# Kernel tuning notes

Measured on AMD Instinct MI355X. Metric: run time of the kernel, lower is better.

Reference implementation:

```python
import jax, jax.numpy as jnp
import numpy as np


def setup_inputs() -> dict:
    key = jax.random.key(0)
    ks = jax.random.split(key, 3)
    B, d_in, d_latent = 8192, 768, 12288
    x = jax.random.normal(ks[0], (B, d_in), dtype=jnp.float32)
    # kaiming_normal fan_in relu: std = sqrt(2/d_in)
    W_enc = jax.random.normal(ks[1], (d_latent, d_in), dtype=jnp.float32) * np.sqrt(2.0 / d_in)
    b_enc = jnp.zeros((d_latent,), dtype=jnp.float32)
    # xavier_normal: std = sqrt(2/(d_in+d_latent))
    W_dec = jax.random.normal(ks[2], (d_in, d_latent), dtype=jnp.float32) * np.sqrt(2.0 / (d_in + d_latent))
    b_dec = jnp.zeros((d_in,), dtype=jnp.float32)
    b_pre = jnp.zeros((d_in,), dtype=jnp.float32)
    return {"x": x, "b_pre": b_pre, "W_enc": W_enc, "b_enc": b_enc,
            "W_dec": W_dec, "b_dec": b_dec, "k": 64}


def reference(x, b_pre, W_enc, b_enc, W_dec, b_dec, k):
    # encode: a = (x - b_pre) @ W_enc.T + b_enc   -> (B, d_latent)
    x0 = x - b_pre
    a = jnp.einsum('bi,li->bl', x0, W_enc) + b_enc
    # topk activation (mode='value', nonneg=True): relu then keep k largest
    a_relu = jax.nn.relu(a)
    topk_val, topk_idx = jax.lax.top_k(a_relu, k)  # (B, k)
    B = a.shape[0]
    rows = jnp.arange(B)[:, None]
    z = jnp.zeros_like(a).at[rows, topk_idx].set(topk_val)
    # decode: x_hat = z @ W_dec.T + b_dec
    x_hat = jnp.einsum('bl,il->bi', z, W_dec) + b_dec
    return (x_hat, z, a)
```

## Files before the change

### kernel.cpp

```cpp
#include <hip/hip_runtime.h>

#define DIN 768
#define DL  12288
#define CAP 320
#define CAP2 512
#define BCAP 2048
#define TCAND 2.9f
#define MARGIN 0.03f
#define UB 0.015f
#define UMAX 64
#define KMAX 128

typedef __attribute__((ext_vector_type(8))) _Float16 half8;
typedef __attribute__((ext_vector_type(4))) _Float16 half4v;
typedef __attribute__((ext_vector_type(4))) float f32x4;

__device__ __forceinline__ void gl_lds16(const void* g, void* s) {
  __builtin_amdgcn_global_load_lds(
      (const __attribute__((address_space(1))) unsigned int*)g,
      (__attribute__((address_space(3))) unsigned int*)s, 16, 0, 0);
}
__device__ __forceinline__ void wait_lgkm0_fence() {
  asm volatile("s_waitcnt lgkmcnt(0)" ::: "memory");
  __builtin_amdgcn_sched_barrier(0);
}
__device__ __forceinline__ void wait_vm0() {
  asm volatile("s_waitcnt vmcnt(0)" ::: "memory");
}

#define NBX (8192 * DIN / 1024)
#define NBW (DL * DIN / 1024)
#define NBT ((DL / 32) * (DIN / 32))

__global__ __launch_bounds__(256) void k_prep(
    const float* __restrict__ x, const float* __restrict__ b_pre,
    const float* __restrict__ W_enc, const float* __restrict__ W_dec,
    _Float16* __restrict__ Ah, _Float16* __restrict__ Bh, _Float16* __restrict__ WT)
{
  const int b = blockIdx.x, tid = threadIdx.x;
  if (b < NBX) {
    const int i4 = b * 256 + tid;
    const int col4 = (i4 % (DIN / 4)) * 4;
    const float4 xv = *(const float4*)&x[(size_t)i4 * 4];
    const float4 bp = *(const float4*)&b_pre[col4];
    half4v o;
    o.x = (_Float16)(xv.x - bp.x);
    o.y = (_Float16)(xv.y - bp.y);
    o.z = (_Float16)(xv.z - bp.z);
    o.w = (_Float16)(xv.w - bp.w);
    *(half4v*)&Ah[(size_t)i4 * 4] = o;
  } else if (b < NBX + NBW) {
    const int i4 = (b - NBX) * 256 + tid;
    const float4 wv = *(const float4*)&W_enc[(size_t)i4 * 4];
    half4v o;
    o.x = (_Float16)wv.x; o.y = (_Float16)wv.y;
    o.z = (_Float16)wv.z; o.w = (_Float16)wv.w;
    *(half4v*)&Bh[(size_t)i4 * 4] = o;
  } else {
    const int idx = b - NBX - NBW;
    const int c0 = (idx % (DL / 32)) * 32;
    const int r0 = (idx / (DL / 32)) * 32;
    const int xx = tid & 31, yy = tid >> 5;
    __shared__ float t[32][33];
#pragma unroll
    for (int dy = 0; dy < 32; dy += 8)
      t[yy + dy][xx] = W_dec[(size_t)(r0 + yy + dy) * DL + c0 + xx];
    __syncthreads();
#pragma unroll
    for (int dy = 0; dy < 32; dy += 8)
      WT[(size_t)(c0 + yy + dy) * DIN + r0 + xx] = (_Float16)t[xx][yy + dy];
  }
}

#define BM 256
#define BN 256
#define BKE 64
#define NKT (DIN / BKE)

template <int EMIT>
__global__ __launch_bounds__(512) void k_encode_f16(
    const _Float16* __restrict__ Ah, const _Float16* __restrict__ Bh,
    const float* __restrict__ b_enc, float* __restrict__ aout,
    int* __restrict__ cnt, int2* __restrict__ cand)
{
  __shared__ _Float16 sA[2][BM][BKE];
  __shared__ _Float16 sB[2][BN][BKE];
  __shared__ int s_bcnt;
  const int tid = threadIdx.x, wave = tid >> 6, lane = tid & 63;
  const int wm = wave >> 2, wn = wave & 3;
  const int fr = lane & 15, fc = lane >> 4;

  const int q = ((8192 / BM) * (DL / BN)) >> 3;
  const int wg = (blockIdx.x & 7) * q + (blockIdx.x >> 3);
  const int bm = (wg / (DL / BN)) * BM;
  const int bn = (wg % (DL / BN)) * BN;

  const int lrow = lane >> 3;
  const int lcol = ((lane & 7) ^ lrow) << 3;
  const _Float16* gA = Ah + (size_t)(bm + lrow) * DIN + lcol;
  const _Float16* gB = Bh + (size_t)(bn + lrow) * DIN + lcol;

  f32x4 acc[8][4];
#pragma unroll
  for (int i = 0; i < 8; ++i)
#pragma unroll
    for (int j = 0; j < 4; ++j) acc[i][j] = f32x4{0.f, 0.f, 0.f, 0.f};

#define STAGE_TILE(buf, tt)                                                      \
  {                                                                              \
    _Pragma("unroll")                                                            \
    for (int s4 = 0; s4 < 4; ++s4) {                                             \
      const int s8 = (wave + s4 * 8) * 8;                                        \
      gl_lds16(gA + (size_t)s8 * DIN + (tt) * BKE, &sA[buf][s8][0]);             \
      gl_lds16(gB + (size_t)s8 * DIN + (tt) * BKE, &sB[buf][s8][0]);             \
    }                                                                            \
  }

#define LOADQ(p, mh, nh)                                                         \
  {                                                                              \
    const char* bA = (const char*)&sA[p][0][0];                                  \
    const char* bB = (const char*)&sB[p][0][0];                                  \
    _Pragma("unroll")                                                            \
    for (int i = 0; i < 4; ++i)                                                  \
      _Pragma("unroll")                                                          \
      for (int ks = 0; ks < 2; ++ks) {                                           \
        const int row = wm * 128 + ((mh) * 4 + i) * 16 + fr;                     \
        const int ph = (ks * 4 + fc) ^ (fr & 7);                                 \
        af[i][ks] = *(const half8*)(bA + row * (BKE * 2) + ph * 16);             \
      }                                                                          \
    _Pragma("unroll")                                                            \
    for (int j = 0; j < 2; ++j)                                                  \
      _Pragma("unroll")                                                          \
      for (int ks = 0; ks < 2; ++ks) {                                           \
        const int row = wn * 64 + ((nh) * 2 + j) * 16 + fr;                      \
        const int ph = (ks * 4 + fc) ^ (fr & 7);                                 \
        bf[j][ks] = *(const half8*)(bB + row * (BKE * 2) + ph * 16);             \
      }                                                                          \
  }

#define MFMAQ(mh, nh)                                                            \
  __builtin_amdgcn_s_setprio(1);                                                 \
  _Pragma("unroll")                                                              \
  for (int i = 0; i < 4; ++i)                                                    \
    _Pragma("unroll")                                                            \
    for (int j = 0; j < 2; ++j)                                                  \
      _Pragma("unroll")                                                          \
      for (int ks = 0; ks < 2; ++ks)                                             \
        acc[(mh) * 4 + i][(nh) * 2 + j] = __builtin_amdgcn_mfma_f32_16x16x32_f16( \
            af[i][ks], bf[j][ks], acc[(mh) * 4 + i][(nh) * 2 + j], 0, 0, 0);     \
  __builtin_amdgcn_s_setprio(0);

  half8 af[4][2], bf[2][2];

  STAGE_TILE(0, 0)
  wait_vm0();
  __builtin_amdgcn_s_barrier();

#pragma unroll 1
  for (int t = 0; t < NKT; ++t) {
    const int p = t & 1;
    LOADQ(p, 0, 0)
    if (t + 1 < NKT) STAGE_TILE(p ^ 1, t + 1)
    __builtin_amdgcn_s_barrier();
    wait_lgkm0_fence();
    MFMAQ(0, 0)
    __builtin_amdgcn_s_barrier();
    LOADQ(p, 0, 1)
    __builtin_amdgcn_s_barrier();
    wait_lgkm0_fence();
    MFMAQ(0, 1)
    __builtin_amdgcn_s_barrier();
    LOADQ(p, 1, 0)
    __builtin_amdgcn_s_barrier();
    wait_lgkm0_fence();
    MFMAQ(1, 0)
    __builtin_amdgcn_s_barrier();
    LOADQ(p, 1, 1)
    wait_vm0();
    __builtin_amdgcn_s_barrier();
    wait_lgkm0_fence();
    MFMAQ(1, 1)
    __builtin_amdgcn_s_barrier();
  }

  unsigned* pk   = (unsigned*)&sA[0][0][0];
  float*    pv   = (float*)&sA[1][0][0];
  int*      lcnt = (int*)&sB[0][0][0];
  if (EMIT) {
    if (tid == 0) s_bcnt = 0;
    if (tid < 256) lcnt[tid] = 0;
    __syncthreads();
  }

#pragma unroll
  for (int j = 0; j < 4; ++j) {
    const int col = bn + wn * 64 + j * 16 + fr;
    const float be = b_enc[col];
#pragma unroll
    for (int i = 0; i < 8; ++i) {
      const int row0 = bm + wm * 128 + i * 16 + fc * 4;
#pragma unroll
      for (int r = 0; r < 4; ++r) {
        const float v = acc[i][j][r] + be;
        aout[(size_t)(row0 + r) * DL + col] = v;
        if (EMIT && v > TCAND) {
          const int lr = wm * 128 + i * 16 + fc * 4 + r;
          const int lc = wn * 64 + j * 16 + fr;
          const int p2 = atomicAdd(&s_bcnt, 1);
          if (p2 < BCAP) {
            pk[p2] = ((unsigned)lr << 8) | (unsigned)lc;
            pv[p2] = v;
          }
          atomicAdd(&lcnt[lr], 1);
        }
      }
    }
  }

  if (EMIT) {
    __syncthreads();
    const int total = s_bcnt;
    if (total > BCAP) {
      if (tid < 256) atomicAdd(&cnt[bm + tid], CAP2);
    } else {
      if (tid < 256) {
        const int c = lcnt[tid];
        lcnt[tid] = c ? atomicAdd(&cnt[bm + tid], c) : 0;
      }
      __syncthreads();
      for (int e = tid; e < total; e += 512) {
        const unsigned pkv = pk[e];
        const int lr = pkv >> 8, lc = pkv & 255u;
        const int p2 = atomicAdd(&lcnt[lr], 1);
        if (p2 < CAP2) {
          int2 o; o.x = __float_as_int(pv[e]); o.y = bn + lc;
          cand[(size_t)(bm + lr) * CAP2 + p2] = o;
        }
      }
    }
  }
#undef STAGE_TILE
#undef LOADQ
#undef MFMAQ
}

__global__ __launch_bounds__(512) void k_fast(
    const int* __restrict__ cnt, const int2* __restrict__ cand,
    const float* __restrict__ x, const float* __restrict__ b_pre,
    const float* __restrict__ W, const float* __restrict__ b_enc,
    const int* __restrict__ kp, const _Float16* __restrict__ WT,
    const float* __restrict__ b_dec, float* __restrict__ z,
    float* __restrict__ xhat, int* __restrict__ flag)
{
  const int row = blockIdx.x, tid = threadIdx.x;
  const int wave = tid >> 6, lane = tid & 63;
  const int kk = min(max(kp[0], 1), KMAX);
  float* zr = z + (size_t)row * DL;

  __shared__ float cv[CAP2];
  __shared__ int ci[CAP2];
  __shared__ double x0[DIN];
  __shared__ float s_ak;
  __shared__ int s_nw, s_ucnt;
  __shared__ int uidx[UMAX];
  __shared__ double uex[UMAX];
  __shared__ int widx[KMAX];
  __shared__ float wval[KMAX];

  const float4 zz = {0.f, 0.f, 0.f, 0.f};
#pragma unroll
  for (int j = 0; j < 6; ++j) ((float4*)zr)[tid + 512 * j] = zz;

  const int Craw = cnt[row];
  const int C = min(Craw, CAP2);
  for (int i = tid; i < C; i += 512) {
    const int2 p = cand[(size_t)row * CAP2 + i];
    cv[i] = __int_as_float(p.x);
    ci[i] = p.y;
  }
  for (int i = tid; i < DIN; i += 512)
    x0[i] = (double)x[(size_t)row * DIN + i] - (double)b_pre[i];
  if (tid == 0) { s_ak = -1e30f; s_nw = 0; s_ucnt = 0; }
  __syncthreads();

  bool defic = (Craw >= CAP2) || (C < kk);
  if (!defic) {
    if (tid < C) {
      const float mv = cv[tid];
      const int mi = ci[tid];
      int r = 0;
      for (int j = 0; j < C; ++j) {
        const float fj = cv[j];
        if (fj > mv || (fj == mv && ci[j] < mi)) ++r;
      }
      if (r == kk - 1) s_ak = mv;
    }
    __syncthreads();
    if (s_ak - UB <= TCAND) defic = true;
  } else {
    __syncthreads();
  }
  if (defic) {
    if (tid == 0) flag[row] = 1;
    return;
  }
  const float ak = s_ak;

  if (tid < C) {
    const float mv = cv[tid];
    if (mv > ak + UB) {
      const int p = atomicAdd(&s_nw, 1);
      widx[p] = ci[tid]; wval[p] = mv;
    } else if (mv >= ak - UB) {
      const int p = atomicAdd(&s_ucnt, 1);
      if (p < UMAX) uidx[p] = ci[tid];
    }
  }
  __syncthreads();
  const int nci = s_nw;
  const int ucnt = min(s_ucnt, UMAX);

  for (int c = wave; c < ucnt; c += 8) {
    const int idx = uidx[c];
    const float* wrow = W + (size_t)idx * DIN;
    double s = 0.0;
#pragma unroll
    for (int it = 0; it < DIN / 64; ++it)
      s = fma(x0[lane + it * 64], (double)wrow[lane + it * 64], s);
#pragma unroll
    for (int mm = 32; mm; mm >>= 1) s += __shfl_xor(s, mm);
    if (lane == 0) {
      const double e = s + (double)b_enc[idx];
      uex[c] = e > 0.0 ? e : 0.0;
    }
  }
  __syncthreads();

  const int utake = min(kk - nci, ucnt);
  if (tid < ucnt) {
    const double mv = uex[tid];
    const int mi = uidx[tid];
    int r = 0;
    for (int j = 0; j < ucnt; ++j) {
      const double fj = uex[j];
      if (fj > mv || (fj == mv && uidx[j] < mi)) ++r;
    }
    if (r < utake) {
      const int p = atomicAdd(&s_nw, 1);
      widx[p] = mi; wval[p] = (float)mv;
    }
  }
  __syncthreads();
  const int nW = s_nw;

  if (tid < nW) zr[widx[tid]] = wval[tid];

  if (tid < 192) {
    float4 acc = ((const float4*)b_dec)[tid];
    for (int j = 0; j < nW; ++j) {
      const float vv = wval[j];
      const half4v w4 = *(const half4v*)(WT + (size_t)widx[j] * DIN + tid * 4);
      acc.x = fmaf(vv, (float)w4.x, acc.x);
      acc.y = fmaf(vv, (float)w4.y, acc.y);
      acc.z = fmaf(vv, (float)w4.z, acc.z);
      acc.w = fmaf(vv, (float)w4.w, acc.w);
    }
    ((float4*)(xhat + (size_t)row * DIN))[tid] = acc;
  }
}

template <int FORCE_ALL, int ZERO_Z>
__global__ __launch_bounds__(512) void k_full(
    const float* __restrict__ a, const float* __restrict__ x,
    const float* __restrict__ b_pre, const float* __restrict__ W,
    const float* __restrict__ b_enc, const int* __restrict__ kp,
    const _Float16* __restrict__ WT, const float* __restrict__ b_dec,
    float* __restrict__ z, float* __restrict__ xhat, const int* __restrict__ flag)
{
  const int row = blockIdx.x, tid = threadIdx.x;
  if (!FORCE_ALL && flag[row] == 0) return;
  const int wave = tid >> 6, lane = tid & 63;
  const int kk = min(max(kp[0], 1), KMAX);
  const float* ar = a + (size_t)row * DL;
  float* zr = z + (size_t)row * DL;

  __shared__ unsigned hist[4][512];
  __shared__ float s_wmax[8];
  __shared__ unsigned s_wsuf[8];
  __shared__ float s_Tm;
  __shared__ int s_cnt;
  __shared__ int cidx[CAP];
  __shared__ float caf[CAP];
  __shared__ double x0[DIN];
  __shared__ float s_ak;
  __shared__ int s_ucnt, s_nw;
  __shared__ int uidx[UMAX];
  __shared__ double uex[UMAX];
  __shared__ int widx[KMAX];
  __shared__ float wval[KMAX];

  float4 v[6];
#pragma unroll
  for (int j = 0; j < 6; ++j) {
    float4 t4 = ((const float4*)ar)[tid + 512 * j];
    t4.x = fmaxf(t4.x, 0.f); t4.y = fmaxf(t4.y, 0.f);
    t4.z = fmaxf(t4.z, 0.f); t4.w = fmaxf(t4.w, 0.f);
    v[j] = t4;
    if (ZERO_Z) {
      const float4 zz = {0.f, 0.f, 0.f, 0.f};
      ((float4*)zr)[tid + 512 * j] = zz;
    }
  }
  for (int i = tid; i < DIN; i += 512)
    x0[i] = (double)x[(size_t)row * DIN + i] - (double)b_pre[i];
  float m = 0.f;
#pragma unroll
  for (int j = 0; j < 6; ++j)
    m = fmaxf(m, fmaxf(fmaxf(v[j].x, v[j].y), fmaxf(v[j].z, v[j].w)));
#pragma unroll
  for (int off = 32; off; off >>= 1) m = fmaxf(m, __shfl_xor(m, off));
  if (lane == 0) s_wmax[wave] = m;
  if (tid == 0) { s_cnt = 0; s_Tm = -1.f; s_ak = -1e30f; s_ucnt = 0; s_nw = 0; }
  __syncthreads();
  float rmax = s_wmax[0];
#pragma unroll
  for (int w2 = 1; w2 < 8; ++w2) rmax = fmaxf(rmax, s_wmax[w2]);

  float Tm;
  if (rmax <= 0.f) {
    Tm = 1e30f;
  } else {
    const float scale = 512.f / rmax;
    unsigned need = (unsigned)kk;
    bool found = false;
    for (int phase = 0; phase < 2 && !found; ++phase) {
      for (int i = tid; i < 4 * 512; i += 512) (&hist[0][0])[i] = 0u;
      __syncthreads();
      unsigned* h = hist[wave & 3];
      const float sc = (phase == 0) ? scale : scale * 8.f;
#pragma unroll
      for (int j = 0; j < 6; ++j) {
        const float vv[4] = {v[j].x, v[j].y, v[j].z, v[j].w};
#pragma unroll
        for (int e = 0; e < 4; ++e) {
          const float val = vv[e];
          if (val > 0.f) {
            const float fb = val * scale;
            if (phase == 0) {
              if (fb >= 64.f) atomicAdd(&h[min(511, (int)fb)], 1u);
            } else {
              if (fb < 64.f) atomicAdd(&h[min(511, (int)(val * sc))], 1u);
            }
          }
        }
      }
      __syncthreads();
      const unsigned st = hist[0][tid] + hist[1][tid] + hist[2][tid] + hist[3][tid];
      unsigned s = st;
#pragma unroll
      for (int off = 1; off < 64; off <<= 1) {
        const unsigned o = __shfl_down(s, off);
        if (lane + off < 64) s += o;
      }
      if (lane == 0) s_wsuf[wave] = s;
      __syncthreads();
      unsigned above_w = 0, total = 0;
#pragma unroll
      for (int w2 = 0; w2 < 8; ++w2) {
        total += s_wsuf[w2];
        if (w2 > wave) above_w += s_wsuf[w2];
      }
      const unsigned inc = s + above_w;
      const unsigned excl = inc - st;
      if (total >= need) {
        if (inc >= need && excl < need)
          s_Tm = (float)tid / sc - MARGIN;
        found = true;
      } else {
        need -= total;
      }
      __syncthreads();
    }
    Tm = s_Tm;
  }

#pragma unroll
  for (int j = 0; j < 6; ++j) {
    const float vv[4] = {v[j].x, v[j].y, v[j].z, v[j].w};
#pragma unroll
    for (int e = 0; e < 4; ++e) {
      if (vv[e] > 0.f && vv[e] >= Tm) {
        const int p = atomicAdd(&s_cnt, 1);
        if (p < CAP) { cidx[p] = (tid + 512 * j) * 4 + e; caf[p] = vv[e]; }
      }
    }
  }
  __syncthreads();
  const int C = min(s_cnt, CAP);

  if (C > kk) {
    if (tid < C) {
      const float mv = caf[tid];
      const int mi = cidx[tid];
      int r = 0;
      for (int j = 0; j < C; ++j) {
        const float fj = caf[j];
        if (fj > mv || (fj == mv && cidx[j] < mi)) ++r;
      }
      if (r == kk - 1) s_ak = mv;
    }
    __syncthreads();
  }
  const float ak = s_ak;

  if (tid < C) {
    const float mv = caf[tid];
    if (C <= kk || mv > ak + UB) {
      const int p = atomicAdd(&s_nw, 1);
      widx[p] = cidx[tid]; wval[p] = mv;
    } else if (mv >= ak - UB) {
      const int p = atomicAdd(&s_ucnt, 1);
      if (p < UMAX) uidx[p] = cidx[tid];
    }
  }
  __syncthreads();
  const int nci = s_nw;
  const int ucnt = min(s_ucnt, UMAX);

  for (int c = wave; c < ucnt; c += 8) {
    const int idx = uidx[c];
    const float* wrow = W + (size_t)idx * DIN;
    double s = 0.0;
#pragma unroll
    for (int it = 0; it < DIN / 64; ++it)
      s = fma(x0[lane + it * 64], (double)wrow[lane + it * 64], s);
#pragma unroll
    for (int mm = 32; mm; mm >>= 1) s += __shfl_xor(s, mm);
    if (lane == 0) {
      const double e = s + (double)b_enc[idx];
      uex[c] = e > 0.0 ? e : 0.0;
    }
  }
  __syncthreads();

  const int utake = min(kk - nci, ucnt);
  if (tid < ucnt) {
    const double mv = uex[tid];
    const int mi = uidx[tid];
    int r = 0;
    for (int j = 0; j < ucnt; ++j) {
      const double fj = uex[j];
      if (fj > mv || (fj == mv && uidx[j] < mi)) ++r;
    }
    if (r < utake) {
      const int p = atomicAdd(&s_nw, 1);
      widx[p] = mi; wval[p] = (float)mv;
    }
  }
  __syncthreads();
  const int nW = s_nw;

  if (tid < nW) zr[widx[tid]] = wval[tid];

  if (tid < 192) {
    float4 acc = ((const float4*)b_dec)[tid];
    for (int j = 0; j < nW; ++j) {
      const float vv = wval[j];
      const half4v w4 = *(const half4v*)(WT + (size_t)widx[j] * DIN + tid * 4);
      acc.x = fmaf(vv, (float)w4.x, acc.x);
      acc.y = fmaf(vv, (float)w4.y, acc.y);
      acc.z = fmaf(vv, (float)w4.z, acc.z);
      acc.w = fmaf(vv, (float)w4.w, acc.w);
    }
    ((float4*)(xhat + (size_t)row * DIN))[tid] = acc;
  }
}

extern "C" void kernel_launch(void* const* d_in, const int* in_sizes, int n_in,
                              void* d_out, int out_size, void* d_ws, size_t ws_size,
                              hipStream_t stream)
{
  const float* x     = (const float*)d_in[0];
  const float* b_pre = (const float*)d_in[1];
  const float* W_enc = (const float*)d_in[2];
  const float* b_enc = (const float*)d_in[3];
  const float* W_dec = (const float*)d_in[4];
  const float* b_dec = (const float*)d_in[5];
  const int*   kp    = (const int*)d_in[6];
  const int M = in_sizes[0] / DIN;

  float* xhat = (float*)d_out;
  float* z    = xhat + (size_t)M * DIN;
  float* a    = z + (size_t)M * DL;

  const bool bigws = ws_size >= ((size_t)192 << 20);

  if (bigws) {
    int*      cnt  = (int*)d_ws;
    int*      flag = (int*)d_ws + M;
    int2*     cand = (int2*)((char*)d_ws + ((size_t)1 << 20));
    _Float16* WT16 = (_Float16*)((char*)d_ws + ((size_t)40 << 20));
    _Float16* Ah   = (_Float16*)((char*)d_ws + ((size_t)64 << 20));
    _Float16* Bh   = (_Float16*)((char*)d_ws + ((size_t)96 << 20));

    hipMemsetAsync(d_ws, 0, 2 * M * sizeof(int), stream);
    k_prep<<<NBX + NBW + NBT, 256, 0, stream>>>(x, b_pre, W_enc, W_dec, Ah, Bh, WT16);
    k_encode_f16<1><<<(M / BM) * (DL / BN), 512, 0, stream>>>(Ah, Bh, b_enc, a, cnt, cand);
    k_fast<<<M, 512, 0, stream>>>(cnt, cand, x, b_pre, W_enc, b_enc, kp, WT16, b_dec,
                                  z, xhat, flag);
    k_full<0, 0><<<M, 512, 0, stream>>>(a, x, b_pre, W_enc, b_enc, kp, WT16, b_dec,
                                        z, xhat, flag);
  } else {
    _Float16* WT16 = (_Float16*)z;
    _Float16* Ah   = (_Float16*)(z + (size_t)12 * 1024 * 1024);
    _Float16* Bh   = (_Float16*)(z + (size_t)20 * 1024 * 1024);

    k_prep<<<NBX + NBW + NBT, 256, 0, stream>>>(x, b_pre, W_enc, W_dec, Ah, Bh, WT16);
    k_encode_f16<0><<<(M / BM) * (DL / BN), 512, 0, stream>>>(Ah, Bh, b_enc, a,
                                                              nullptr, nullptr);
    k_full<1, 1><<<M, 512, 0, stream>>>(a, x, b_pre, W_enc, b_enc, kp, WT16, b_dec,
                                        z, xhat, nullptr);
  }
}
```

Before: 661.2 us.

## Move z zeroing into encode GEMM prologue and fold counter memset into prep

The dense zeroing of z moves out of the per-row k_fast kernel. Each encode GEMM block now writes zeros for its own 256x256 tile of z during the prologue, overlapped with the first tile's global-to-LDS loads through a partial vmcnt wait. The separate hipMemsetAsync of the count/flag array is replaced by one extra k_prep block that zeroes it, removing an API call. The risk is that the GEMM's extra stores compete for bandwidth with its operand loads, and the vmcnt(32) wait must correctly cover the staged loads.

```diff
diff --git a/kernel.cpp b/kernel.cpp
--- a/kernel.cpp
+++ b/kernel.cpp
@@ -32,10 +32,12 @@
 #define NBW (DL * DIN / 1024)
 #define NBT ((DL / 32) * (DIN / 32))
 
+template <int ZMETA>
 __global__ __launch_bounds__(256) void k_prep(
     const float* __restrict__ x, const float* __restrict__ b_pre,
     const float* __restrict__ W_enc, const float* __restrict__ W_dec,
-    _Float16* __restrict__ Ah, _Float16* __restrict__ Bh, _Float16* __restrict__ WT)
+    _Float16* __restrict__ Ah, _Float16* __restrict__ Bh, _Float16* __restrict__ WT,
+    int* __restrict__ meta)
 {
   const int b = blockIdx.x, tid = threadIdx.x;
   if (b < NBX) {
@@ -56,7 +58,7 @@
     o.x = (_Float16)wv.x; o.y = (_Float16)wv.y;
     o.z = (_Float16)wv.z; o.w = (_Float16)wv.w;
     *(half4v*)&Bh[(size_t)i4 * 4] = o;
-  } else {
+  } else if (b < NBX + NBW + NBT) {
     const int idx = b - NBX - NBW;
     const int c0 = (idx % (DL / 32)) * 32;
     const int r0 = (idx / (DL / 32)) * 32;
@@ -69,6 +71,10 @@
 #pragma unroll
     for (int dy = 0; dy < 32; dy += 8)
       WT[(size_t)(c0 + yy + dy) * DIN + r0 + xx] = (_Float16)t[xx][yy + dy];
+  } else if (ZMETA) {
+    const int4 z4 = {0, 0, 0, 0};
+#pragma unroll
+    for (int s = 0; s < 16; ++s) ((int4*)meta)[tid * 16 + s] = z4;
   }
 }
 
@@ -81,7 +87,7 @@
 __global__ __launch_bounds__(512) void k_encode_f16(
     const _Float16* __restrict__ Ah, const _Float16* __restrict__ Bh,
     const float* __restrict__ b_enc, float* __restrict__ aout,
-    int* __restrict__ cnt, int2* __restrict__ cand)
+    int* __restrict__ cnt, int2* __restrict__ cand, float* __restrict__ zout)
 {
   __shared__ _Float16 sA[2][BM][BKE];
   __shared__ _Float16 sB[2][BN][BKE];
@@ -153,7 +159,15 @@
   half8 af[4][2], bf[2][2];
 
   STAGE_TILE(0, 0)
-  wait_vm0();
+  if (EMIT) {
+    const float4 zz4 = {0.f, 0.f, 0.f, 0.f};
+#pragma unroll
+    for (int s = 0; s < 32; ++s)
+      *(float4*)&zout[(size_t)(bm + s * 8 + wave) * DL + bn + lane * 4] = zz4;
+    asm volatile("s_waitcnt vmcnt(32)" ::: "memory");
+  } else {
+    wait_vm0();
+  }
   __builtin_amdgcn_s_barrier();
 
 #pragma unroll 1
@@ -266,10 +280,6 @@
   __shared__ double uex[UMAX];
   __shared__ int widx[KMAX];
   __shared__ float wval[KMAX];
-
-  const float4 zz = {0.f, 0.f, 0.f, 0.f};
-#pragma unroll
-  for (int j = 0; j < 6; ++j) ((float4*)zr)[tid + 512 * j] = zz;
 
   const int Craw = cnt[row];
   const int C = min(Craw, CAP2);
@@ -603,9 +613,10 @@
     _Float16* Ah   = (_Float16*)((char*)d_ws + ((size_t)64 << 20));
     _Float16* Bh   = (_Float16*)((char*)d_ws + ((size_t)96 << 20));
 
-    hipMemsetAsync(d_ws, 0, 2 * M * sizeof(int), stream);
-    k_prep<<<NBX + NBW + NBT, 256, 0, stream>>>(x, b_pre, W_enc, W_dec, Ah, Bh, WT16);
-    k_encode_f16<1><<<(M / BM) * (DL / BN), 512, 0, stream>>>(Ah, Bh, b_enc, a, cnt, cand);
+    k_prep<1><<<NBX + NBW + NBT + 1, 256, 0, stream>>>(x, b_pre, W_enc, W_dec,
+                                                       Ah, Bh, WT16, cnt);
+    k_encode_f16<1><<<(M / BM) * (DL / BN), 512, 0, stream>>>(Ah, Bh, b_enc, a,
+                                                              cnt, cand, z);
     k_fast<<<M, 512, 0, stream>>>(cnt, cand, x, b_pre, W_enc, b_enc, kp, WT16, b_dec,
                                   z, xhat, flag);
     k_full<0, 0><<<M, 512, 0, stream>>>(a, x, b_pre, W_enc, b_enc, kp, WT16, b_dec,
@@ -615,9 +626,10 @@
     _Float16* Ah   = (_Float16*)(z + (size_t)12 * 1024 * 1024);
     _Float16* Bh   = (_Float16*)(z + (size_t)20 * 1024 * 1024);
 
-    k_prep<<<NBX + NBW + NBT, 256, 0, stream>>>(x, b_pre, W_enc, W_dec, Ah, Bh, WT16);
+    k_prep<0><<<NBX + NBW + NBT, 256, 0, stream>>>(x, b_pre, W_enc, W_dec,
+                                                   Ah, Bh, WT16, nullptr);
     k_encode_f16<0><<<(M / BM) * (DL / BN), 512, 0, stream>>>(Ah, Bh, b_enc, a,
-                                                              nullptr, nullptr);
+                                                              nullptr, nullptr, nullptr);
     k_full<1, 1><<<M, 512, 0, stream>>>(a, x, b_pre, W_enc, b_enc, kp, WT16, b_dec,
                                         z, xhat, nullptr);
   }
```

New measurement: 700.6 us. 1.06x slower.
